# Performance work log

Hardware: AMD Instinct MI355X
Metric: run time of the kernel (lower is better)

## Reference

```python
import jax, jax.numpy as jnp
import numpy as np

B, S, T, E, H = 2, 2048, 2048, 1024, 16
D = E // H  # head_dim = 64


def setup_inputs() -> dict:
    key = jax.random.key(0)
    ks = jax.random.split(key, 11)
    scale = 1.0 / np.sqrt(E)
    return {
        "query": jax.random.normal(ks[0], (B, S, E), jnp.float32),
        "value": jax.random.normal(ks[1], (B, T, E), jnp.float32),
        "key": jax.random.normal(ks[2], (B, T, E), jnp.float32),
        "Wq": jax.random.normal(ks[3], (E, E), jnp.float32) * scale,
        "bq": jnp.zeros((E,), jnp.float32),
        "Wk": jax.random.normal(ks[4], (E, E), jnp.float32) * scale,
        "bk": jnp.zeros((E,), jnp.float32),
        "Wv": jax.random.normal(ks[5], (E, E), jnp.float32) * scale,
        "bv": jnp.zeros((E,), jnp.float32),
        "Wo": jax.random.normal(ks[6], (E, E), jnp.float32) * scale,
        "bo": jnp.zeros((E,), jnp.float32),
    }


def reference(query, value, key, Wq, bq, Wk, bk, Wv, bv, Wo, bo):
    b, s, e = query.shape
    t = value.shape[1]
    # linear projections (torch Linear: x @ W.T + b)
    q = query @ Wq.T + bq
    k = key @ Wk.T + bk
    v = value @ Wv.T + bv
    # split heads: [B, H, S, D]
    q = q.reshape(b, s, H, D).transpose(0, 2, 1, 3)
    k = k.reshape(b, t, H, D).transpose(0, 2, 1, 3)
    v = v.reshape(b, t, H, D).transpose(0, 2, 1, 3)
    # scaled dot-product attention; full [B,H,S,T] scores as in the original
    A = jnp.einsum("bhsd,bhtd->bhst", q, k) / jnp.sqrt(jnp.float32(D))
    A = jax.nn.softmax(A, axis=-1)
    # dropout p=0.0 -> identity
    out = jnp.einsum("bhst,bhtd->bhsd", A, v)
    out = out.transpose(0, 2, 1, 3).reshape(b, s, e)
    return out @ Wo.T + bo
```

## Files before the change

kernel.cpp:

```cpp
#include <hip/hip_runtime.h>
#include <math.h>

typedef __attribute__((ext_vector_type(8))) short short8;
typedef __attribute__((ext_vector_type(4))) float f32x4;
typedef unsigned short u16;

__device__ __forceinline__ u16 f2bf(float x) {
    unsigned int u = __float_as_uint(x);
    u += 0x7FFFu + ((u >> 16) & 1u);
    return (u16)(u >> 16);
}

__device__ __forceinline__ unsigned cvt_pk_bf16(float lo, float hi) {
    unsigned r;
    asm("v_cvt_pk_bf16_f32 %0, %1, %2" : "=v"(r) : "v"(lo), "v"(hi));
    return r;
}

__device__ __forceinline__ void load_lds16(const void* g, void* l) {
    __builtin_amdgcn_global_load_lds(
        (const __attribute__((address_space(1))) unsigned int*)g,
        (__attribute__((address_space(3))) unsigned int*)l,
        16, 0, 0);
}

struct CvtArgs {
    const float* src[7];
    u16* dst[7];
    int n8[7];
};

__global__ __launch_bounds__(256) void cvt_bf16(CvtArgs c) {
    const int z = blockIdx.z;
    const int i = blockIdx.x * 256 + threadIdx.x;
    if (i >= c.n8[z]) return;
    const float4* s = (const float4*)c.src[z];
    const float4 a = s[2 * i];
    const float4 b = s[2 * i + 1];
    union { short8 v; unsigned u[4]; } o;
    o.u[0] = cvt_pk_bf16(a.x, a.y);
    o.u[1] = cvt_pk_bf16(a.z, a.w);
    o.u[2] = cvt_pk_bf16(b.x, b.y);
    o.u[3] = cvt_pk_bf16(b.z, b.w);
    ((short8*)c.dst[z])[i] = o.v;
}

struct GemmArgs {
    const u16* A[3];
    const u16* W[3];
    const float* bias[3];
    void* C[3];
    float scale[3];
    int trans[3];
};

template <bool BF16OUT>
__global__ __launch_bounds__(256) void gemm_nt_mfma(GemmArgs ga, int M, int N, int K)
{
    __shared__ u16 As[128 * 32];
    __shared__ u16 Bs[128 * 32];
    const int z = blockIdx.z;
    const u16* __restrict__ A = ga.A[z];
    const u16* __restrict__ W = ga.W[z];
    const float* __restrict__ bias = ga.bias[z];
    const float scale = ga.scale[z];
    const int trans = ga.trans[z];

    const int tid = threadIdx.x;
    const int w = tid >> 6, l = tid & 63;
    const int l4 = l >> 4, lm = l & 15;
    const int wr = w >> 1, wc = w & 1;

    const int idx = blockIdx.x;
    const int xcd = idx & 7;
    const int sl  = idx >> 3;
    const int bmi = xcd * 4 + (sl & 3);
    const int bni = sl >> 2;
    const int bm = (trans ? bni : bmi) * 128;
    const int bn = (trans ? bmi : bni) * 128;

    const int srow = l >> 2;
    const int sseg = l & 3;

    f32x4 acc[4][4];
#pragma unroll
    for (int m = 0; m < 4; ++m)
#pragma unroll
        for (int n = 0; n < 4; ++n) acc[m][n] = (f32x4){0.f, 0.f, 0.f, 0.f};

    for (int k0 = 0; k0 < K; k0 += 32) {
        __syncthreads();
#pragma unroll
        for (int i = 0; i < 2; ++i) {
            const int blk = w * 2 + i;
            const int row = blk * 16 + srow;
            load_lds16(A + (size_t)(bm + row) * K + k0 + sseg * 8,
                       (char*)As + blk * 1024);
            load_lds16(W + (size_t)(bn + row) * K + k0 + sseg * 8,
                       (char*)Bs + blk * 1024);
        }
        __syncthreads();

        short8 af[4], bf[4];
#pragma unroll
        for (int m = 0; m < 4; ++m)
            af[m] = *(const short8*)&As[(wr * 64 + m * 16 + lm) * 32 + l4 * 8];
#pragma unroll
        for (int n = 0; n < 4; ++n)
            bf[n] = *(const short8*)&Bs[(wc * 64 + n * 16 + lm) * 32 + l4 * 8];
#pragma unroll
        for (int m = 0; m < 4; ++m)
#pragma unroll
            for (int n = 0; n < 4; ++n)
                acc[m][n] = __builtin_amdgcn_mfma_f32_16x16x32_bf16(af[m], bf[n], acc[m][n], 0, 0, 0);
    }

    if (!trans) {
        float bv[4];
#pragma unroll
        for (int n = 0; n < 4; ++n) bv[n] = bias[bn + wc * 64 + n * 16 + lm];
#pragma unroll
        for (int m = 0; m < 4; ++m) {
#pragma unroll
            for (int n = 0; n < 4; ++n) {
                const int col = bn + wc * 64 + n * 16 + lm;
#pragma unroll
                for (int r = 0; r < 4; ++r) {
                    const int row = bm + wr * 64 + m * 16 + l4 * 4 + r;
                    const float v = (acc[m][n][r] + bv[n]) * scale;
                    if (BF16OUT)
                        ((u16*)ga.C[z])[(size_t)row * N + col] = f2bf(v);
                    else
                        ((float*)ga.C[z])[(size_t)row * N + col] = v;
                }
            }
        }
    } else {
#pragma unroll
        for (int m = 0; m < 4; ++m) {
            const float4 bv4 = *(const float4*)(bias + bm + wr * 64 + m * 16 + l4 * 4);
            const float bvr[4] = {bv4.x, bv4.y, bv4.z, bv4.w};
#pragma unroll
            for (int n = 0; n < 4; ++n) {
                const int col = bn + wc * 64 + n * 16 + lm;
                const size_t cbase = (size_t)(col >> 11) * 2097152 + (size_t)(col & 2047);
#pragma unroll
                for (int r = 0; r < 4; ++r) {
                    const int row = bm + wr * 64 + m * 16 + l4 * 4 + r;
                    const float v = (acc[m][n][r] + bvr[r]) * scale;
                    ((u16*)ga.C[z])[cbase + (size_t)row * 2048] = f2bf(v);
                }
            }
        }
    }
}

__global__ __launch_bounds__(512, 4) void flash_attn_mfma6(
    const u16* __restrict__ Qb, const u16* __restrict__ Kb,
    const u16* __restrict__ Vt, u16* __restrict__ Ob)
{
    __shared__ u16 Ks[2][128 * 64];
    __shared__ u16 Vs[2][64 * 128];
    __shared__ u16 Ps[8][16 * 64];

    const int tid = threadIdx.x;
    const int w  = tid >> 6;
    const int l  = tid & 63;
    const int l4 = l >> 4;
    const int lm = l & 15;

    const int id = blockIdx.x;
    const int xcd = id & 7;
    const int s = id >> 3;
    const int qt = s & 15;
    const int g0 = (s >> 4) * 8 + xcd;
    const int h = g0 & 15;
    const int b = g0 >> 4;
    const int qb0 = qt << 7;

    const size_t bbase = (size_t)b * 2048 * 1024 + (size_t)h * 64;
    const size_t vbase = (size_t)b * 2097152 + (size_t)(h * 64) * 2048;

    short8 qf[2];
    {
        const u16* qrow = Qb + bbase + (size_t)(qb0 + w * 16 + lm) * 1024;
        qf[0] = *(const short8*)(qrow + l4 * 8);
        qf[1] = *(const short8*)(qrow + 32 + l4 * 8);
    }

    auto stageK = [&](int t0, int bufi) {
#pragma unroll
        for (int ii = 0; ii < 2; ++ii) {
            const int i = w * 2 + ii;
            const int key = i * 8 + (l >> 3);
            const int chunk = (l & 7) ^ ((l >> 3) & 7);
            load_lds16(Kb + bbase + (size_t)(t0 + key) * 1024 + chunk * 8,
                       (char*)&Ks[bufi][0] + i * 1024);
        }
    };
    auto stageV = [&](int t0, int bufi) {
#pragma unroll
        for (int ii = 0; ii < 2; ++ii) {
            const int i = w * 2 + ii;
            const int d = i * 4 + (l >> 4);
            const int chunk = (l & 15) ^ (d & 7);
            load_lds16(Vt + vbase + (size_t)d * 2048 + t0 + chunk * 8,
                       (char*)&Vs[bufi][0] + i * 1024);
        }
    };

    f32x4 oacc[4];
#pragma unroll
    for (int g = 0; g < 4; ++g) oacc[g] = (f32x4){0.f, 0.f, 0.f, 0.f};
    float m_run = -1e30f;
    float l_run = 0.f;

    stageK(0, 0);
    stageV(0, 0);
    __syncthreads();

    for (int t = 0; t < 16; ++t) {
        const int buf = t & 1;
        if (t < 15) {
            stageK((t + 1) * 128, buf ^ 1);
            stageV((t + 1) * 128, buf ^ 1);
        }

        f32x4 sacc[8];
#pragma unroll
        for (int g = 0; g < 8; ++g) sacc[g] = (f32x4){0.f, 0.f, 0.f, 0.f};
        __builtin_amdgcn_s_setprio(1);
#pragma unroll
        for (int g = 0; g < 8; ++g) {
#pragma unroll
            for (int c = 0; c < 2; ++c) {
                const short8 kf = *(const short8*)
                    &Ks[buf][(16 * g + lm) * 64 + (((4 * c + l4) ^ (lm & 7)) << 3)];
                sacc[g] = __builtin_amdgcn_mfma_f32_16x16x32_bf16(kf, qf[c], sacc[g], 0, 0, 0);
            }
        }
        __builtin_amdgcn_s_setprio(0);

        float amax[8];
#pragma unroll
        for (int g = 0; g < 8; ++g)
            amax[g] = fmaxf(fmaxf(sacc[g][0], sacc[g][1]), fmaxf(sacc[g][2], sacc[g][3]));
        float mt = fmaxf(fmaxf(fmaxf(amax[0], amax[1]), fmaxf(amax[2], amax[3])),
                         fmaxf(fmaxf(amax[4], amax[5]), fmaxf(amax[6], amax[7])));
        mt = fmaxf(mt, __shfl_xor(mt, 16));
        mt = fmaxf(mt, __shfl_xor(mt, 32));

        const bool resc = !__all(mt <= m_run);
        if (resc) {
            const float mn = fmaxf(m_run, mt);
            const float alpha = __builtin_amdgcn_exp2f(m_run - mn);
            m_run = mn;
            l_run *= alpha;
#pragma unroll
            for (int r = 0; r < 4; ++r) {
                const float a = __shfl(alpha, l4 * 4 + r);
#pragma unroll
                for (int g = 0; g < 4; ++g) oacc[g][r] *= a;
            }
        }

        float lsum = 0.f;
        const float mr = m_run;
#pragma unroll
        for (int hh = 0; hh < 2; ++hh) {
#pragma unroll
            for (int gg = 0; gg < 4; ++gg) {
                const int g = hh * 4 + gg;
                const float p0 = __builtin_amdgcn_exp2f(sacc[g][0] - mr);
                const float p1 = __builtin_amdgcn_exp2f(sacc[g][1] - mr);
                const float p2 = __builtin_amdgcn_exp2f(sacc[g][2] - mr);
                const float p3 = __builtin_amdgcn_exp2f(sacc[g][3] - mr);
                lsum += (p0 + p1) + (p2 + p3);
                uint2 pk;
                pk.x = cvt_pk_bf16(p0, p1);
                pk.y = cvt_pk_bf16(p2, p3);
                *(uint2*)&Ps[w][lm * 64 + (((gg * 4 + l4) ^ ((lm & 7) << 1)) << 2)] = pk;
            }
            __builtin_amdgcn_s_setprio(1);
#pragma unroll
            for (int c = 0; c < 2; ++c) {
                const short8 pa = *(const short8*)
                    &Ps[w][lm * 64 + (((c * 8 + l4 * 2) ^ ((lm & 7) << 1)) << 2)];
#pragma unroll
                for (int g = 0; g < 4; ++g) {
                    const int d = 16 * g + lm;
                    const short8 vf = *(const short8*)
                        &Vs[buf][d * 128 + (((hh * 8 + c * 4 + l4) ^ (d & 7)) << 3)];
                    oacc[g] = __builtin_amdgcn_mfma_f32_16x16x32_bf16(pa, vf, oacc[g], 0, 0, 0);
                }
            }
            __builtin_amdgcn_s_setprio(0);
        }
        lsum += __shfl_xor(lsum, 16);
        lsum += __shfl_xor(lsum, 32);
        l_run += lsum;

        __syncthreads();
    }

#pragma unroll
    for (int r = 0; r < 4; ++r) {
        const float linv = 1.f / __shfl(l_run, l4 * 4 + r);
        const size_t orow = bbase + (size_t)(qb0 + w * 16 + l4 * 4 + r) * 1024;
#pragma unroll
        for (int g = 0; g < 4; ++g)
            Ob[orow + g * 16 + lm] = f2bf(oacc[g][r] * linv);
    }
}

extern "C" void kernel_launch(void* const* d_in, const int* in_sizes, int n_in,
                              void* d_out, int out_size, void* d_ws, size_t ws_size,
                              hipStream_t stream)
{
    const float* query = (const float*)d_in[0];
    const float* value = (const float*)d_in[1];
    const float* key   = (const float*)d_in[2];
    const float* Wq = (const float*)d_in[3];
    const float* bq = (const float*)d_in[4];
    const float* Wk = (const float*)d_in[5];
    const float* bk = (const float*)d_in[6];
    const float* Wv = (const float*)d_in[7];
    const float* bv = (const float*)d_in[8];
    const float* Wo = (const float*)d_in[9];
    const float* bo = (const float*)d_in[10];
    float* out = (float*)d_out;

    const int M = 2 * 2048;
    const int E = 1024;
    const size_t act = (size_t)M * E;
    const size_t wel = (size_t)E * E;

    u16* qc  = (u16*)d_ws;
    u16* kc  = qc + act;
    u16* vc  = kc + act;
    u16* wqb = vc + act;
    u16* wkb = wqb + wel;
    u16* wvb = wkb + wel;
    u16* wob = wvb + wel;
    u16* Qb  = wob + wel;
    u16* Kb  = Qb + act;
    u16* Vtb = Kb + act;
    u16* Ab  = Vtb + act;

    CvtArgs ca;
    ca.src[0] = query; ca.dst[0] = qc;  ca.n8[0] = (int)(act / 8);
    ca.src[1] = key;   ca.dst[1] = kc;  ca.n8[1] = (int)(act / 8);
    ca.src[2] = value; ca.dst[2] = vc;  ca.n8[2] = (int)(act / 8);
    ca.src[3] = Wq;    ca.dst[3] = wqb; ca.n8[3] = (int)(wel / 8);
    ca.src[4] = Wk;    ca.dst[4] = wkb; ca.n8[4] = (int)(wel / 8);
    ca.src[5] = Wv;    ca.dst[5] = wvb; ca.n8[5] = (int)(wel / 8);
    ca.src[6] = Wo;    ca.dst[6] = wob; ca.n8[6] = (int)(wel / 8);
    dim3 cgrid((unsigned)((act / 8 + 255) / 256), 1, 7);
    hipLaunchKernelGGL(cvt_bf16, cgrid, dim3(256), 0, stream, ca);

    const float SCALE_Q = 0.125f * 1.4426950408889634f;

    GemmArgs gq;
    gq.A[0] = qc;  gq.W[0] = wqb; gq.bias[0] = bq; gq.C[0] = Qb;  gq.scale[0] = SCALE_Q; gq.trans[0] = 0;
    gq.A[1] = kc;  gq.W[1] = wkb; gq.bias[1] = bk; gq.C[1] = Kb;  gq.scale[1] = 1.0f;    gq.trans[1] = 0;
    gq.A[2] = wvb; gq.W[2] = vc;  gq.bias[2] = bv; gq.C[2] = Vtb; gq.scale[2] = 1.0f;    gq.trans[2] = 1;
    hipLaunchKernelGGL((gemm_nt_mfma<true>), dim3(256, 1, 3), dim3(256), 0, stream, gq, M, E, E);

    hipLaunchKernelGGL(flash_attn_mfma6, dim3(512), dim3(512), 0, stream, Qb, Kb, Vtb, Ab);

    GemmArgs go;
    go.A[0] = Ab; go.W[0] = wob; go.bias[0] = bo; go.C[0] = out; go.scale[0] = 1.0f; go.trans[0] = 0;
    go.A[1] = Ab; go.W[1] = wob; go.bias[1] = bo; go.C[1] = out; go.scale[1] = 1.0f; go.trans[1] = 0;
    go.A[2] = Ab; go.W[2] = wob; go.bias[2] = bo; go.C[2] = out; go.scale[2] = 1.0f; go.trans[2] = 0;
    hipLaunchKernelGGL((gemm_nt_mfma<false>), dim3(256, 1, 1), dim3(256), 0, stream, go, M, E, E);
}
```

Measured before the change: 149.7 us.

## Keep softmax probabilities in registers via permlane swaps, add lazy rescale threshold

Replaces the per-wave LDS round-trip for the P tile (write bf16 probabilities to shared memory, read back as MFMA A-operands) with v_permlane32/16_swap instructions that rearrange the packed bf16 values across lanes in registers. This removes LDS traffic and the shared Ps buffer. It also makes the online-softmax rescale lazy, skipping it unless the new max exceeds the running max by more than 8 (log2 units). That cuts rescale work but lets unnormalized exponentials grow up to 2^8, with some precision risk.

```diff
diff --git a/kernel.cpp b/kernel.cpp
--- a/kernel.cpp
+++ b/kernel.cpp
@@ -155,13 +155,12 @@
     }
 }
 
-__global__ __launch_bounds__(512, 4) void flash_attn_mfma6(
+__global__ __launch_bounds__(512, 4) void flash_attn_mfma7(
     const u16* __restrict__ Qb, const u16* __restrict__ Kb,
     const u16* __restrict__ Vt, u16* __restrict__ Ob)
 {
     __shared__ u16 Ks[2][128 * 64];
     __shared__ u16 Vs[2][64 * 128];
-    __shared__ u16 Ps[8][16 * 64];
 
     const int tid = threadIdx.x;
     const int w  = tid >> 6;
@@ -250,7 +249,7 @@
         mt = fmaxf(mt, __shfl_xor(mt, 16));
         mt = fmaxf(mt, __shfl_xor(mt, 32));
 
-        const bool resc = !__all(mt <= m_run);
+        const bool resc = !__all(mt <= m_run + 8.0f);
         if (resc) {
             const float mn = fmaxf(m_run, mt);
             const float alpha = __builtin_amdgcn_exp2f(m_run - mn);
@@ -266,39 +265,41 @@
 
         float lsum = 0.f;
         const float mr = m_run;
-#pragma unroll
-        for (int hh = 0; hh < 2; ++hh) {
-#pragma unroll
-            for (int gg = 0; gg < 4; ++gg) {
-                const int g = hh * 4 + gg;
-                const float p0 = __builtin_amdgcn_exp2f(sacc[g][0] - mr);
-                const float p1 = __builtin_amdgcn_exp2f(sacc[g][1] - mr);
-                const float p2 = __builtin_amdgcn_exp2f(sacc[g][2] - mr);
-                const float p3 = __builtin_amdgcn_exp2f(sacc[g][3] - mr);
-                lsum += (p0 + p1) + (p2 + p3);
-                uint2 pk;
-                pk.x = cvt_pk_bf16(p0, p1);
-                pk.y = cvt_pk_bf16(p2, p3);
-                *(uint2*)&Ps[w][lm * 64 + (((gg * 4 + l4) ^ ((lm & 7) << 1)) << 2)] = pk;
-            }
-            __builtin_amdgcn_s_setprio(1);
-#pragma unroll
-            for (int c = 0; c < 2; ++c) {
-                const short8 pa = *(const short8*)
-                    &Ps[w][lm * 64 + (((c * 8 + l4 * 2) ^ ((lm & 7) << 1)) << 2)];
-#pragma unroll
-                for (int g = 0; g < 4; ++g) {
-                    const int d = 16 * g + lm;
-                    const short8 vf = *(const short8*)
-                        &Vs[buf][d * 128 + (((hh * 8 + c * 4 + l4) ^ (d & 7)) << 3)];
-                    oacc[g] = __builtin_amdgcn_mfma_f32_16x16x32_bf16(pa, vf, oacc[g], 0, 0, 0);
-                }
-            }
-            __builtin_amdgcn_s_setprio(0);
+        unsigned up[8], vp[8];
+#pragma unroll
+        for (int g = 0; g < 8; ++g) {
+            const float p0 = __builtin_amdgcn_exp2f(sacc[g][0] - mr);
+            const float p1 = __builtin_amdgcn_exp2f(sacc[g][1] - mr);
+            const float p2 = __builtin_amdgcn_exp2f(sacc[g][2] - mr);
+            const float p3 = __builtin_amdgcn_exp2f(sacc[g][3] - mr);
+            lsum += (p0 + p1) + (p2 + p3);
+            up[g] = cvt_pk_bf16(p0, p1);
+            vp[g] = cvt_pk_bf16(p2, p3);
         }
         lsum += __shfl_xor(lsum, 16);
         lsum += __shfl_xor(lsum, 32);
         l_run += lsum;
+
+#pragma unroll
+        for (int kb = 0; kb < 4; ++kb) {
+            unsigned w0 = up[2 * kb], w2 = up[2 * kb + 1];
+            unsigned w1 = vp[2 * kb], w3 = vp[2 * kb + 1];
+            asm("v_permlane32_swap_b32 %0, %1" : "+v"(w0), "+v"(w2));
+            asm("v_permlane16_swap_b32 %0, %1" : "+v"(w0), "+v"(w2));
+            asm("v_permlane32_swap_b32 %0, %1" : "+v"(w1), "+v"(w3));
+            asm("v_permlane16_swap_b32 %0, %1" : "+v"(w1), "+v"(w3));
+            union { unsigned u[4]; short8 v8; } pa;
+            pa.u[0] = w0; pa.u[1] = w1; pa.u[2] = w2; pa.u[3] = w3;
+            __builtin_amdgcn_s_setprio(1);
+#pragma unroll
+            for (int g = 0; g < 4; ++g) {
+                const int d = 16 * g + lm;
+                const short8 vf = *(const short8*)
+                    &Vs[buf][d * 128 + (((kb * 4 + l4) ^ (d & 7)) << 3)];
+                oacc[g] = __builtin_amdgcn_mfma_f32_16x16x32_bf16(pa.v8, vf, oacc[g], 0, 0, 0);
+            }
+            __builtin_amdgcn_s_setprio(0);
+        }
 
         __syncthreads();
     }
@@ -366,7 +367,7 @@
     gq.A[2] = wvb; gq.W[2] = vc;  gq.bias[2] = bv; gq.C[2] = Vtb; gq.scale[2] = 1.0f;    gq.trans[2] = 1;
     hipLaunchKernelGGL((gemm_nt_mfma<true>), dim3(256, 1, 3), dim3(256), 0, stream, gq, M, E, E);
 
-    hipLaunchKernelGGL(flash_attn_mfma6, dim3(512), dim3(512), 0, stream, Qb, Kb, Vtb, Ab);
+    hipLaunchKernelGGL(flash_attn_mfma7, dim3(512), dim3(512), 0, stream, Qb, Kb, Vtb, Ab);
 
     GemmArgs go;
     go.A[0] = Ab; go.W[0] = wob; go.bias[0] = bo; go.C[0] = out; go.scale[0] = 1.0f; go.trans[0] = 0;
```

Result: no change. 146.9 us (-1.9%).
